# Performance work log

Hardware: AMD Instinct MI355X
Metric: run time of the kernel (lower is better)

The kernel has to match this reference:

```python
import jax, jax.numpy as jnp
import numpy as np

EPS = 1e-5

def rmsnorm(x, g):
    var = jnp.mean(jnp.square(x), axis=-1, keepdims=True)
    return x * jax.lax.rsqrt(var + EPS) * g

def setup_inputs() -> dict:
    key = jax.random.key(0)
    ks = jax.random.split(key, 8)
    B, S, T, D = 2, 2048, 2048, 1024
    H, HKV, HD = 16, 4, 64
    std = 0.02
    return {
        "x": jax.random.normal(ks[0], (B, S, D), jnp.float32),
        "kv": jax.random.normal(ks[1], (B, T, D), jnp.float32),
        "wq": jax.random.normal(ks[2], (H * HD, D), jnp.float32) * std,
        "wk": jax.random.normal(ks[3], (HKV * HD, D), jnp.float32) * std,
        "wv": jax.random.normal(ks[4], (HKV * HD, D), jnp.float32) * std,
        "wo": jax.random.normal(ks[5], (D, H * HD), jnp.float32) * std,
        "gq": jnp.ones((D,), jnp.float32),
        "gkv": jnp.ones((D,), jnp.float32),
    }

def reference(x, kv, wq, wk, wv, wo, gq, gkv):
    B, S, D = x.shape
    T = kv.shape[1]
    H, HKV, HD = 16, 4, 64
    R = H // HKV  # heads per kv group
    xn = rmsnorm(x, gq)
    kvn = rmsnorm(kv, gkv)
    # projections
    q = (xn @ wq.T).reshape(B, S, HKV, R, HD)   # grouped query heads
    k = (kvn @ wk.T).reshape(B, T, HKV, HD)
    v = (kvn @ wv.T).reshape(B, T, HKV, HD)
    scale = 1.0 / jnp.sqrt(jnp.float32(HD))
    # block-mask is None -> full dense cross attention; GQA via broadcast einsum
    scores = jnp.einsum('bsgrd,btgd->bgrst', q, k) * scale  # [B,HKV,R,S,T]
    probs = jax.nn.softmax(scores, axis=-1)
    out = jnp.einsum('bgrst,btgd->bsgrd', probs, v)  # [B,S,HKV,R,HD]
    out = out.reshape(B, S, H * HD) @ wo.T
    return x + out
```

## Files before the change

### kernel.cpp

```cpp
#include <hip/hip_runtime.h>

#define DEV __device__ __forceinline__

typedef __attribute__((ext_vector_type(8))) short frag8;
typedef __attribute__((ext_vector_type(8))) _Float16 h8;
typedef __attribute__((ext_vector_type(4))) float f32x4;

DEV unsigned short f2bf(float f) {
  union { float f; unsigned int u; } v; v.f = f;
  unsigned int r = v.u + 0x7fffu + ((v.u >> 16) & 1u);
  return (unsigned short)(r >> 16);
}

DEV unsigned short f2h(float f) {
  union { _Float16 h[2]; unsigned short u[2]; } v;
  v.h[0] = (_Float16)f;
  return v.u[0];
}

DEV float h2f(unsigned short u) {
  union { _Float16 h[2]; unsigned short u[2]; } v;
  v.u[0] = u;
  return (float)v.h[0];
}

DEV unsigned int pack2h(float a, float b) {
  union { __fp16 __attribute__((ext_vector_type(2))) p; unsigned int u; } v;
  v.p = __builtin_amdgcn_cvt_pkrtz(a, b);
  return v.u;
}

DEV void async_load16(const void* g, void* l) {
  __builtin_amdgcn_global_load_lds(
      (const __attribute__((address_space(1))) void*)g,
      (__attribute__((address_space(3))) void*)l,
      16, 0, 0);
}

__global__ __launch_bounds__(256) void fused_cast(const float* __restrict__ wq,
                                                  const float* __restrict__ wk,
                                                  const float* __restrict__ wv,
                                                  const float* __restrict__ wo,
                                                  unsigned short* __restrict__ wqb,
                                                  unsigned short* __restrict__ wkvb,
                                                  unsigned short* __restrict__ wob,
                                                  float qscale) {
  const int b = blockIdx.x;
  const float* src;
  unsigned short* dst;
  float sc = 1.0f;
  int base;
  if (b < 1024) { src = wq; dst = wqb; sc = qscale; base = b; }
  else if (b < 1280) { src = wk; dst = wkvb; base = b - 1024; }
  else if (b < 1536) { src = wv; dst = wkvb + 262144; base = b - 1280; }
  else { src = wo; dst = wob; base = b - 1536; }
  const int i = (base * 256 + threadIdx.x) * 4;
  float4 v = *(const float4*)&src[i];
  ushort4 o;
  o.x = f2bf(v.x * sc); o.y = f2bf(v.y * sc);
  o.z = f2bf(v.z * sc); o.w = f2bf(v.w * sc);
  *(ushort4*)&dst[i] = o;
}

__global__ __launch_bounds__(256) void rmsnorm2(const float* __restrict__ x,
                                                const float* __restrict__ kv,
                                                const float* __restrict__ gq,
                                                const float* __restrict__ gkv,
                                                unsigned short* __restrict__ xn,
                                                unsigned short* __restrict__ kvn) {
  int row = blockIdx.x;
  const int tid = threadIdx.x;
  const float* src;
  const float* g;
  unsigned short* dst;
  if (row < 4096) { src = x; g = gq; dst = xn; }
  else { row -= 4096; src = kv; g = gkv; dst = kvn; }
  const float* xr = src + (size_t)row * 1024;
  float4 v = *(const float4*)&xr[tid * 4];
  float ss = v.x * v.x + v.y * v.y + v.z * v.z + v.w * v.w;
  ss += __shfl_xor(ss, 32); ss += __shfl_xor(ss, 16);
  ss += __shfl_xor(ss, 8);  ss += __shfl_xor(ss, 4);
  ss += __shfl_xor(ss, 2);  ss += __shfl_xor(ss, 1);
  __shared__ float red[4];
  if ((tid & 63) == 0) red[tid >> 6] = ss;
  __syncthreads();
  float tot = red[0] + red[1] + red[2] + red[3];
  float inv = rsqrtf(tot * (1.0f / 1024.0f) + 1e-5f);
  float4 gv = *(const float4*)&g[tid * 4];
  ushort4 o;
  o.x = f2bf(v.x * inv * gv.x); o.y = f2bf(v.y * inv * gv.y);
  o.z = f2bf(v.z * inv * gv.z); o.w = f2bf(v.w * inv * gv.w);
  *(ushort4*)&dst[(size_t)row * 1024 + tid * 4] = o;
}

template <int BM, int BN, int MODE>
__global__ __launch_bounds__(256) void gemm_bt(const unsigned short* __restrict__ A,
                                               const unsigned short* __restrict__ W,
                                               void* __restrict__ out,
                                               const float* __restrict__ resid,
                                               unsigned short* __restrict__ out2,
                                               int M, int N, int K) {
  constexpr int MI = BM / 32, NI = BN / 32;
  constexpr int PA = BM / 32, PB = BN / 32;
  __shared__ unsigned short Al[2][2][BM * 32];
  __shared__ unsigned short Bl[2][2][BN * 32];
  const int tid = threadIdx.x;
  const int w = tid >> 6, l = tid & 63;
  const int quad = l >> 4, ln = l & 15;
  const int m0 = blockIdx.y * BM, n0 = blockIdx.x * BN;
  const int wm0 = (w >> 1) * (MI * 16), wn0 = (w & 1) * (NI * 16);
  const int r4 = l >> 2;
  const int c4 = (l & 3) * 8;

  f32x4 acc[MI][NI] = {};

  auto stage = [&](int buf, int kk) {
#pragma unroll
    for (int j = 0; j < PA; ++j) {
      const int idx = w * PA + j;
      const int p = idx / (BM / 16), c = idx % (BM / 16);
      async_load16(A + (size_t)(m0 + c * 16 + r4) * K + kk + p * 32 + c4,
                   &Al[buf][p][c * 512]);
    }
#pragma unroll
    for (int j = 0; j < PB; ++j) {
      const int idx = w * PB + j;
      const int p = idx / (BN / 16), c = idx % (BN / 16);
      async_load16(W + (size_t)(n0 + c * 16 + r4) * K + kk + p * 32 + c4,
                   &Bl[buf][p][c * 512]);
    }
  };

  stage(0, 0);
  const int iters = K >> 6;
#pragma unroll 2
  for (int it = 0; it < iters; ++it) {
    const int buf = it & 1;
    __syncthreads();
    if (it + 1 < iters) stage(buf ^ 1, (it + 1) << 6);
#pragma unroll
    for (int kc = 0; kc < 2; ++kc) {
      frag8 af[MI], bfr[NI];
#pragma unroll
      for (int mi = 0; mi < MI; ++mi)
        af[mi] = *(const frag8*)&Al[buf][kc][(wm0 + mi * 16 + ln) * 32 + quad * 8];
#pragma unroll
      for (int ni = 0; ni < NI; ++ni)
        bfr[ni] = *(const frag8*)&Bl[buf][kc][(wn0 + ni * 16 + ln) * 32 + quad * 8];
#pragma unroll
      for (int mi = 0; mi < MI; ++mi)
#pragma unroll
        for (int ni = 0; ni < NI; ++ni)
          acc[mi][ni] = __builtin_amdgcn_mfma_f32_16x16x32_bf16(af[mi], bfr[ni], acc[mi][ni], 0, 0, 0);
    }
  }

#pragma unroll
  for (int mi = 0; mi < MI; ++mi) {
#pragma unroll
    for (int ni = 0; ni < NI; ++ni) {
#pragma unroll
      for (int r = 0; r < 4; ++r) {
        const int row = m0 + wm0 + mi * 16 + quad * 4 + r;
        const int col = n0 + wn0 + ni * 16 + ln;
        const float v = acc[mi][ni][r];
        if (MODE == 0) {
          ((unsigned short*)out)[(size_t)row * N + col] = f2bf(v);
        } else if (MODE == 2) {
          const size_t idx = (size_t)row * N + col;
          ((float*)out)[idx] = resid[idx] + v;
        } else {
          if (col < 256) {
            ((unsigned short*)out)[(size_t)row * 256 + col] = f2bf(v);
          } else {
            const int c2 = col - 256, gg = c2 >> 6, dd = c2 & 63;
            const int bb = row >> 11, t = row & 2047;
            out2[((size_t)((bb * 4 + gg) * 64 + dd) << 11) + t] = f2h(v);
          }
        }
      }
    }
  }
}

__global__ __launch_bounds__(256, 4) void flash_attn(const unsigned short* __restrict__ q,
                                                     const unsigned short* __restrict__ k,
                                                     const unsigned short* __restrict__ vT,
                                                     unsigned short* __restrict__ o0,
                                                     unsigned short* __restrict__ o1,
                                                     float* __restrict__ l0p,
                                                     float* __restrict__ l1p) {
  __shared__ unsigned short KV[4][64 * 32];
  __shared__ unsigned short P[4 * 32 * 72];

  const int tid = threadIdx.x;
  const int w = tid >> 6, l = tid & 63;
  const int quad = l >> 4, ln = l & 15;
  const int s0 = blockIdx.x * 128;
  const int h = blockIdx.y, g = h >> 2;
  const int b = blockIdx.z >> 1, ts = blockIdx.z & 1;
  const int tbase = ts << 10;

  unsigned short* Opart = ts ? o1 : o0;
  float* lpart = ts ? l1p : l0p;

  frag8 qf[2][2];
#pragma unroll
  for (int nq = 0; nq < 2; ++nq)
#pragma unroll
    for (int c = 0; c < 2; ++c)
      qf[nq][c] = *(const frag8*)&q[(((size_t)(b * 2048 + s0 + w * 32 + nq * 16 + ln)) << 10) +
                                    h * 64 + c * 32 + quad * 8];

  f32x4 oacc[2][4] = {};
  float lsum[2] = {0.0f, 0.0f};

  const unsigned short* kbase = k + ((size_t)(b * 2048)) * 256 + g * 64;
  const unsigned short* vbase = vT + (((size_t)(b * 4 + g) * 64) << 11);
  unsigned short* Pw = &P[w * 32 * 72];

  const int r4 = l >> 2;
  const int c4 = (l & 3) * 8;

  for (int it = 0; it < 16; ++it) {
    const int t0 = tbase + it * 64;
    __syncthreads();
#pragma unroll
    for (int c = 0; c < 4; ++c) {
      const unsigned short* src;
      if (w < 2)
        src = kbase + (size_t)(t0 + c * 16 + r4) * 256 + w * 32 + c4;
      else
        src = vbase + (((size_t)(c * 16 + r4)) << 11) + t0 + (w - 2) * 32 + c4;
      async_load16(src, &KV[w][c * 512]);
    }
    __syncthreads();

    f32x4 st[2][4];
#pragma unroll
    for (int tb = 0; tb < 4; ++tb) {
      frag8 ka = *(const frag8*)&KV[0][(tb * 16 + ln) * 32 + quad * 8];
      frag8 kb2 = *(const frag8*)&KV[1][(tb * 16 + ln) * 32 + quad * 8];
#pragma unroll
      for (int nq = 0; nq < 2; ++nq) {
        f32x4 s = {};
        s = __builtin_amdgcn_mfma_f32_16x16x32_bf16(ka, qf[nq][0], s, 0, 0, 0);
        s = __builtin_amdgcn_mfma_f32_16x16x32_bf16(kb2, qf[nq][1], s, 0, 0, 0);
        st[nq][tb] = s;
      }
    }

#pragma unroll
    for (int nq = 0; nq < 2; ++nq) {
#pragma unroll
      for (int tb = 0; tb < 4; ++tb) {
        float p0 = __builtin_amdgcn_exp2f(fminf(st[nq][tb][0], 14.0f));
        float p1 = __builtin_amdgcn_exp2f(fminf(st[nq][tb][1], 14.0f));
        float p2 = __builtin_amdgcn_exp2f(fminf(st[nq][tb][2], 14.0f));
        float p3 = __builtin_amdgcn_exp2f(fminf(st[nq][tb][3], 14.0f));
        lsum[nq] += (p0 + p1) + (p2 + p3);
        uint2 pk; pk.x = pack2h(p0, p1); pk.y = pack2h(p2, p3);
        *(uint2*)&Pw[(nq * 16 + ln) * 72 + tb * 16 + quad * 4] = pk;
      }
    }

    asm volatile("s_waitcnt lgkmcnt(0)" ::: "memory");

#pragma unroll
    for (int c = 0; c < 2; ++c) {
      h8 pf0 = *(const h8*)&Pw[(0 * 16 + ln) * 72 + c * 32 + quad * 8];
      h8 pf1 = *(const h8*)&Pw[(1 * 16 + ln) * 72 + c * 32 + quad * 8];
#pragma unroll
      for (int cb = 0; cb < 4; ++cb) {
        h8 vb = *(const h8*)&KV[2 + c][(cb * 16 + ln) * 32 + quad * 8];
        oacc[0][cb] = __builtin_amdgcn_mfma_f32_16x16x32_f16(pf0, vb, oacc[0][cb], 0, 0, 0);
        oacc[1][cb] = __builtin_amdgcn_mfma_f32_16x16x32_f16(pf1, vb, oacc[1][cb], 0, 0, 0);
      }
    }
  }

#pragma unroll
  for (int nq = 0; nq < 2; ++nq) {
    lsum[nq] += __shfl_xor(lsum[nq], 16);
    lsum[nq] += __shfl_xor(lsum[nq], 32);
    if (l < 16)
      lpart[(size_t)(b * 2048 + s0 + w * 32 + nq * 16 + l) * 16 + h] = lsum[nq];
#pragma unroll
    for (int r = 0; r < 4; ++r) {
      const size_t row = (size_t)(b * 2048 + s0 + w * 32 + nq * 16 + quad * 4 + r);
#pragma unroll
      for (int cb = 0; cb < 4; ++cb)
        Opart[(row << 10) + h * 64 + cb * 16 + ln] = f2h(oacc[nq][cb][r]);
    }
  }
}

__global__ __launch_bounds__(256) void combine(const unsigned short* __restrict__ O0,
                                               const unsigned short* __restrict__ O1,
                                               const float* __restrict__ l0p,
                                               const float* __restrict__ l1p,
                                               unsigned short* __restrict__ att) {
  const int row = blockIdx.x, tid = threadIdx.x;
  const int col = tid * 4;
  const int h = tid >> 4;
  const float inv = 1.0f / (l0p[row * 16 + h] + l1p[row * 16 + h]);
  const size_t idx = ((size_t)row << 10) + col;
  ushort4 a = *(const ushort4*)&O0[idx];
  ushort4 b = *(const ushort4*)&O1[idx];
  ushort4 o;
  o.x = f2bf((h2f(a.x) + h2f(b.x)) * inv);
  o.y = f2bf((h2f(a.y) + h2f(b.y)) * inv);
  o.z = f2bf((h2f(a.z) + h2f(b.z)) * inv);
  o.w = f2bf((h2f(a.w) + h2f(b.w)) * inv);
  *(ushort4*)&att[idx] = o;
}

extern "C" void kernel_launch(void* const* d_in, const int* in_sizes, int n_in,
                              void* d_out, int out_size, void* d_ws, size_t ws_size,
                              hipStream_t stream) {
  const float* x   = (const float*)d_in[0];
  const float* kv  = (const float*)d_in[1];
  const float* wq  = (const float*)d_in[2];
  const float* wk  = (const float*)d_in[3];
  const float* wv  = (const float*)d_in[4];
  const float* wo  = (const float*)d_in[5];
  const float* gq  = (const float*)d_in[6];
  const float* gkv = (const float*)d_in[7];

  char* ws = (char*)d_ws;
  unsigned short* xn   = (unsigned short*)(ws);
  unsigned short* kvn  = (unsigned short*)(ws + 8388608);
  unsigned short* qb   = (unsigned short*)(ws + 16777216);
  unsigned short* kb   = (unsigned short*)(ws + 25165824);
  unsigned short* vTb  = (unsigned short*)(ws + 27262976);
  unsigned short* attb = (unsigned short*)(ws + 29360128);
  unsigned short* wqb  = (unsigned short*)(ws + 37748736);
  unsigned short* wkvb = (unsigned short*)(ws + 39845888);
  unsigned short* wob  = (unsigned short*)(ws + 40894464);
  unsigned short* Opart0 = xn;
  unsigned short* Opart1 = kvn;
  float* l0p = (float*)wqb;
  float* l1p = (float*)(ws + 37748736 + 262144);

  const float qscale = 0.18033688011112042f;
  fused_cast<<<2560, 256, 0, stream>>>(wq, wk, wv, wo, wqb, wkvb, wob, qscale);
  rmsnorm2<<<8192, 256, 0, stream>>>(x, kv, gq, gkv, xn, kvn);

  gemm_bt<64, 64, 0><<<dim3(16, 64), 256, 0, stream>>>(xn, wqb, qb, nullptr, nullptr,
                                                       4096, 1024, 1024);
  gemm_bt<64, 64, 3><<<dim3(8, 64), 256, 0, stream>>>(kvn, wkvb, kb, nullptr, vTb,
                                                      4096, 512, 1024);

  flash_attn<<<dim3(16, 16, 4), 256, 0, stream>>>(qb, kb, vTb, Opart0, Opart1, l0p, l1p);
  combine<<<4096, 256, 0, stream>>>(Opart0, Opart1, l0p, l1p, attb);

  gemm_bt<64, 64, 2><<<dim3(16, 64), 256, 0, stream>>>(attb, wob, d_out, x, nullptr,
                                                       4096, 1024, 1024);
}
```

Measured before the change: 204.1 us.

## Split-K 128x128 projection GEMMs with fp16 partials and larger flash-attention query tiles

Replaces the 64x64 Q and output projection GEMMs with a 128x128-tile split-K kernel. Each half of K writes fp16 partials; the Q partials are summed inside the attention prologue and the output partials are summed in a new residual-add kernel. K is now stored as fp16, and the QK^T MFMAs switch from bf16 to f16. Flash attention now processes 256 query rows per block, 64 per wave, with the exp applied directly after each score MFMA, and its occupancy hint drops from 4 to 2. The larger tiles aim to raise data reuse, but they cost an extra combine pass, a single-buffered GEMM main loop, fewer resident blocks, and a small loss of precision from the fp16 partial sums.

```diff
diff --git a/kernel.cpp b/kernel.cpp
--- a/kernel.cpp
+++ b/kernel.cpp
@@ -93,97 +93,139 @@
   *(ushort4*)&dst[(size_t)row * 1024 + tid * 4] = o;
 }
 
-template <int BM, int BN, int MODE>
-__global__ __launch_bounds__(256) void gemm_bt(const unsigned short* __restrict__ A,
+__global__ __launch_bounds__(256) void gemm_fat(const unsigned short* __restrict__ A,
+                                                const unsigned short* __restrict__ W,
+                                                unsigned short* __restrict__ p0,
+                                                unsigned short* __restrict__ p1) {
+  __shared__ unsigned short Al[2][128 * 32];
+  __shared__ unsigned short Bl[2][128 * 32];
+  const int tid = threadIdx.x;
+  const int w = tid >> 6, l = tid & 63;
+  const int quad = l >> 4, ln = l & 15;
+  const int m0 = blockIdx.y * 128, n0 = blockIdx.x * 128;
+  const int kb0 = blockIdx.z * 512;
+  unsigned short* part = blockIdx.z ? p1 : p0;
+  const int wm0 = (w >> 1) * 64, wn0 = (w & 1) * 64;
+  const int r4 = l >> 2;
+  const int c4 = (l & 3) * 8;
+
+  f32x4 acc[4][4] = {};
+
+  for (int kk = 0; kk < 512; kk += 64) {
+    __syncthreads();
+#pragma unroll
+    for (int j = 0; j < 4; ++j) {
+      const int idx = w * 4 + j;
+      const int p = idx >> 3, rb = (idx & 7) * 16;
+      async_load16(A + (size_t)(m0 + rb + r4) * 1024 + kb0 + kk + p * 32 + c4,
+                   &Al[p][rb * 32]);
+      async_load16(W + (size_t)(n0 + rb + r4) * 1024 + kb0 + kk + p * 32 + c4,
+                   &Bl[p][rb * 32]);
+    }
+    __syncthreads();
+#pragma unroll
+    for (int kc = 0; kc < 2; ++kc) {
+      frag8 af[4], bf[4];
+#pragma unroll
+      for (int mi = 0; mi < 4; ++mi)
+        af[mi] = *(const frag8*)&Al[kc][(wm0 + mi * 16 + ln) * 32 + quad * 8];
+#pragma unroll
+      for (int ni = 0; ni < 4; ++ni)
+        bf[ni] = *(const frag8*)&Bl[kc][(wn0 + ni * 16 + ln) * 32 + quad * 8];
+#pragma unroll
+      for (int mi = 0; mi < 4; ++mi)
+#pragma unroll
+        for (int ni = 0; ni < 4; ++ni)
+          acc[mi][ni] = __builtin_amdgcn_mfma_f32_16x16x32_bf16(af[mi], bf[ni], acc[mi][ni], 0, 0, 0);
+    }
+  }
+
+#pragma unroll
+  for (int mi = 0; mi < 4; ++mi)
+#pragma unroll
+    for (int ni = 0; ni < 4; ++ni)
+#pragma unroll
+      for (int r = 0; r < 4; ++r) {
+        const int row = m0 + wm0 + mi * 16 + quad * 4 + r;
+        const int col = n0 + wn0 + ni * 16 + ln;
+        part[((size_t)row << 10) + col] = f2h(acc[mi][ni][r]);
+      }
+}
+
+__global__ __launch_bounds__(256) void gemm_kv(const unsigned short* __restrict__ A,
                                                const unsigned short* __restrict__ W,
-                                               void* __restrict__ out,
-                                               const float* __restrict__ resid,
-                                               unsigned short* __restrict__ out2,
-                                               int M, int N, int K) {
-  constexpr int MI = BM / 32, NI = BN / 32;
-  constexpr int PA = BM / 32, PB = BN / 32;
+                                               unsigned short* __restrict__ kout,
+                                               unsigned short* __restrict__ vout) {
+  constexpr int BM = 64, BN = 64;
   __shared__ unsigned short Al[2][2][BM * 32];
   __shared__ unsigned short Bl[2][2][BN * 32];
   const int tid = threadIdx.x;
   const int w = tid >> 6, l = tid & 63;
   const int quad = l >> 4, ln = l & 15;
   const int m0 = blockIdx.y * BM, n0 = blockIdx.x * BN;
-  const int wm0 = (w >> 1) * (MI * 16), wn0 = (w & 1) * (NI * 16);
+  const int wm0 = (w >> 1) * 32, wn0 = (w & 1) * 32;
   const int r4 = l >> 2;
   const int c4 = (l & 3) * 8;
-
-  f32x4 acc[MI][NI] = {};
+  const int K = 1024;
+
+  f32x4 acc[2][2] = {};
 
   auto stage = [&](int buf, int kk) {
 #pragma unroll
-    for (int j = 0; j < PA; ++j) {
-      const int idx = w * PA + j;
-      const int p = idx / (BM / 16), c = idx % (BM / 16);
+    for (int j = 0; j < 2; ++j) {
+      const int idx = w * 2 + j;
+      const int p = idx >> 2, c = idx & 3;
       async_load16(A + (size_t)(m0 + c * 16 + r4) * K + kk + p * 32 + c4,
                    &Al[buf][p][c * 512]);
-    }
-#pragma unroll
-    for (int j = 0; j < PB; ++j) {
-      const int idx = w * PB + j;
-      const int p = idx / (BN / 16), c = idx % (BN / 16);
       async_load16(W + (size_t)(n0 + c * 16 + r4) * K + kk + p * 32 + c4,
                    &Bl[buf][p][c * 512]);
     }
   };
 
   stage(0, 0);
-  const int iters = K >> 6;
 #pragma unroll 2
-  for (int it = 0; it < iters; ++it) {
+  for (int it = 0; it < 16; ++it) {
     const int buf = it & 1;
     __syncthreads();
-    if (it + 1 < iters) stage(buf ^ 1, (it + 1) << 6);
+    if (it < 15) stage(buf ^ 1, (it + 1) << 6);
 #pragma unroll
     for (int kc = 0; kc < 2; ++kc) {
-      frag8 af[MI], bfr[NI];
-#pragma unroll
-      for (int mi = 0; mi < MI; ++mi)
+      frag8 af[2], bf[2];
+#pragma unroll
+      for (int mi = 0; mi < 2; ++mi)
         af[mi] = *(const frag8*)&Al[buf][kc][(wm0 + mi * 16 + ln) * 32 + quad * 8];
 #pragma unroll
-      for (int ni = 0; ni < NI; ++ni)
-        bfr[ni] = *(const frag8*)&Bl[buf][kc][(wn0 + ni * 16 + ln) * 32 + quad * 8];
-#pragma unroll
-      for (int mi = 0; mi < MI; ++mi)
-#pragma unroll
-        for (int ni = 0; ni < NI; ++ni)
-          acc[mi][ni] = __builtin_amdgcn_mfma_f32_16x16x32_bf16(af[mi], bfr[ni], acc[mi][ni], 0, 0, 0);
+      for (int ni = 0; ni < 2; ++ni)
+        bf[ni] = *(const frag8*)&Bl[buf][kc][(wn0 + ni * 16 + ln) * 32 + quad * 8];
+#pragma unroll
+      for (int mi = 0; mi < 2; ++mi)
+#pragma unroll
+        for (int ni = 0; ni < 2; ++ni)
+          acc[mi][ni] = __builtin_amdgcn_mfma_f32_16x16x32_bf16(af[mi], bf[ni], acc[mi][ni], 0, 0, 0);
     }
   }
 
 #pragma unroll
-  for (int mi = 0; mi < MI; ++mi) {
-#pragma unroll
-    for (int ni = 0; ni < NI; ++ni) {
+  for (int mi = 0; mi < 2; ++mi)
+#pragma unroll
+    for (int ni = 0; ni < 2; ++ni)
 #pragma unroll
       for (int r = 0; r < 4; ++r) {
         const int row = m0 + wm0 + mi * 16 + quad * 4 + r;
         const int col = n0 + wn0 + ni * 16 + ln;
         const float v = acc[mi][ni][r];
-        if (MODE == 0) {
-          ((unsigned short*)out)[(size_t)row * N + col] = f2bf(v);
-        } else if (MODE == 2) {
-          const size_t idx = (size_t)row * N + col;
-          ((float*)out)[idx] = resid[idx] + v;
+        if (col < 256) {
+          kout[(size_t)row * 256 + col] = f2h(v);
         } else {
-          if (col < 256) {
-            ((unsigned short*)out)[(size_t)row * 256 + col] = f2bf(v);
-          } else {
-            const int c2 = col - 256, gg = c2 >> 6, dd = c2 & 63;
-            const int bb = row >> 11, t = row & 2047;
-            out2[((size_t)((bb * 4 + gg) * 64 + dd) << 11) + t] = f2h(v);
-          }
+          const int c2 = col - 256, gg = c2 >> 6, dd = c2 & 63;
+          const int bb = row >> 11, t = row & 2047;
+          vout[((size_t)((bb * 4 + gg) * 64 + dd) << 11) + t] = f2h(v);
         }
       }
-    }
-  }
-}
-
-__global__ __launch_bounds__(256, 4) void flash_attn(const unsigned short* __restrict__ q,
+}
+
+__global__ __launch_bounds__(256, 2) void flash_attn(const unsigned short* __restrict__ qp0,
+                                                     const unsigned short* __restrict__ qp1,
                                                      const unsigned short* __restrict__ k,
                                                      const unsigned short* __restrict__ vT,
                                                      unsigned short* __restrict__ o0,
@@ -191,12 +233,12 @@
                                                      float* __restrict__ l0p,
                                                      float* __restrict__ l1p) {
   __shared__ unsigned short KV[4][64 * 32];
-  __shared__ unsigned short P[4 * 32 * 72];
+  __shared__ unsigned short P[4 * 64 * 72];
 
   const int tid = threadIdx.x;
   const int w = tid >> 6, l = tid & 63;
   const int quad = l >> 4, ln = l & 15;
-  const int s0 = blockIdx.x * 128;
+  const int s0 = blockIdx.x * 256;
   const int h = blockIdx.y, g = h >> 2;
   const int b = blockIdx.z >> 1, ts = blockIdx.z & 1;
   const int tbase = ts << 10;
@@ -204,20 +246,22 @@
   unsigned short* Opart = ts ? o1 : o0;
   float* lpart = ts ? l1p : l0p;
 
-  frag8 qf[2][2];
-#pragma unroll
-  for (int nq = 0; nq < 2; ++nq)
-#pragma unroll
-    for (int c = 0; c < 2; ++c)
-      qf[nq][c] = *(const frag8*)&q[(((size_t)(b * 2048 + s0 + w * 32 + nq * 16 + ln)) << 10) +
-                                    h * 64 + c * 32 + quad * 8];
-
-  f32x4 oacc[2][4] = {};
-  float lsum[2] = {0.0f, 0.0f};
+  h8 qf[4][2];
+#pragma unroll
+  for (int nq = 0; nq < 4; ++nq)
+#pragma unroll
+    for (int c = 0; c < 2; ++c) {
+      const size_t off = (((size_t)(b * 2048 + s0 + w * 64 + nq * 16 + ln)) << 10) +
+                         h * 64 + c * 32 + quad * 8;
+      qf[nq][c] = *(const h8*)&qp0[off] + *(const h8*)&qp1[off];
+    }
+
+  f32x4 oacc[4][4] = {};
+  float lsum[4] = {0.0f, 0.0f, 0.0f, 0.0f};
 
   const unsigned short* kbase = k + ((size_t)(b * 2048)) * 256 + g * 64;
   const unsigned short* vbase = vT + (((size_t)(b * 4 + g) * 64) << 11);
-  unsigned short* Pw = &P[w * 32 * 72];
+  unsigned short* Pw = &P[w * 64 * 72];
 
   const int r4 = l >> 2;
   const int c4 = (l & 3) * 8;
@@ -236,28 +280,19 @@
     }
     __syncthreads();
 
-    f32x4 st[2][4];
 #pragma unroll
     for (int tb = 0; tb < 4; ++tb) {
-      frag8 ka = *(const frag8*)&KV[0][(tb * 16 + ln) * 32 + quad * 8];
-      frag8 kb2 = *(const frag8*)&KV[1][(tb * 16 + ln) * 32 + quad * 8];
-#pragma unroll
-      for (int nq = 0; nq < 2; ++nq) {
+      h8 ka = *(const h8*)&KV[0][(tb * 16 + ln) * 32 + quad * 8];
+      h8 kb2 = *(const h8*)&KV[1][(tb * 16 + ln) * 32 + quad * 8];
+#pragma unroll
+      for (int nq = 0; nq < 4; ++nq) {
         f32x4 s = {};
-        s = __builtin_amdgcn_mfma_f32_16x16x32_bf16(ka, qf[nq][0], s, 0, 0, 0);
-        s = __builtin_amdgcn_mfma_f32_16x16x32_bf16(kb2, qf[nq][1], s, 0, 0, 0);
-        st[nq][tb] = s;
-      }
-    }
-
-#pragma unroll
-    for (int nq = 0; nq < 2; ++nq) {
-#pragma unroll
-      for (int tb = 0; tb < 4; ++tb) {
-        float p0 = __builtin_amdgcn_exp2f(fminf(st[nq][tb][0], 14.0f));
-        float p1 = __builtin_amdgcn_exp2f(fminf(st[nq][tb][1], 14.0f));
-        float p2 = __builtin_amdgcn_exp2f(fminf(st[nq][tb][2], 14.0f));
-        float p3 = __builtin_amdgcn_exp2f(fminf(st[nq][tb][3], 14.0f));
+        s = __builtin_amdgcn_mfma_f32_16x16x32_f16(ka, qf[nq][0], s, 0, 0, 0);
+        s = __builtin_amdgcn_mfma_f32_16x16x32_f16(kb2, qf[nq][1], s, 0, 0, 0);
+        float p0 = __builtin_amdgcn_exp2f(fminf(s[0], 14.0f));
+        float p1 = __builtin_amdgcn_exp2f(fminf(s[1], 14.0f));
+        float p2 = __builtin_amdgcn_exp2f(fminf(s[2], 14.0f));
+        float p3 = __builtin_amdgcn_exp2f(fminf(s[3], 14.0f));
         lsum[nq] += (p0 + p1) + (p2 + p3);
         uint2 pk; pk.x = pack2h(p0, p1); pk.y = pack2h(p2, p3);
         *(uint2*)&Pw[(nq * 16 + ln) * 72 + tb * 16 + quad * 4] = pk;
@@ -268,26 +303,29 @@
 
 #pragma unroll
     for (int c = 0; c < 2; ++c) {
-      h8 pf0 = *(const h8*)&Pw[(0 * 16 + ln) * 72 + c * 32 + quad * 8];
-      h8 pf1 = *(const h8*)&Pw[(1 * 16 + ln) * 72 + c * 32 + quad * 8];
+      h8 pf[4];
+#pragma unroll
+      for (int nq = 0; nq < 4; ++nq)
+        pf[nq] = *(const h8*)&Pw[(nq * 16 + ln) * 72 + c * 32 + quad * 8];
 #pragma unroll
       for (int cb = 0; cb < 4; ++cb) {
         h8 vb = *(const h8*)&KV[2 + c][(cb * 16 + ln) * 32 + quad * 8];
-        oacc[0][cb] = __builtin_amdgcn_mfma_f32_16x16x32_f16(pf0, vb, oacc[0][cb], 0, 0, 0);
-        oacc[1][cb] = __builtin_amdgcn_mfma_f32_16x16x32_f16(pf1, vb, oacc[1][cb], 0, 0, 0);
+#pragma unroll
+        for (int nq = 0; nq < 4; ++nq)
+          oacc[nq][cb] = __builtin_amdgcn_mfma_f32_16x16x32_f16(pf[nq], vb, oacc[nq][cb], 0, 0, 0);
       }
     }
   }
 
 #pragma unroll
-  for (int nq = 0; nq < 2; ++nq) {
+  for (int nq = 0; nq < 4; ++nq) {
     lsum[nq] += __shfl_xor(lsum[nq], 16);
     lsum[nq] += __shfl_xor(lsum[nq], 32);
     if (l < 16)
-      lpart[(size_t)(b * 2048 + s0 + w * 32 + nq * 16 + l) * 16 + h] = lsum[nq];
+      lpart[(size_t)(b * 2048 + s0 + w * 64 + nq * 16 + l) * 16 + h] = lsum[nq];
 #pragma unroll
     for (int r = 0; r < 4; ++r) {
-      const size_t row = (size_t)(b * 2048 + s0 + w * 32 + nq * 16 + quad * 4 + r);
+      const size_t row = (size_t)(b * 2048 + s0 + w * 64 + nq * 16 + quad * 4 + r);
 #pragma unroll
       for (int cb = 0; cb < 4; ++cb)
         Opart[(row << 10) + h * 64 + cb * 16 + ln] = f2h(oacc[nq][cb][r]);
@@ -315,6 +353,23 @@
   *(ushort4*)&att[idx] = o;
 }
 
+__global__ __launch_bounds__(256) void o_combine(const float* __restrict__ x,
+                                                 const unsigned short* __restrict__ p0,
+                                                 const unsigned short* __restrict__ p1,
+                                                 float* __restrict__ out) {
+  const int row = blockIdx.x, tid = threadIdx.x;
+  const size_t idx = ((size_t)row << 10) + tid * 4;
+  float4 xv = *(const float4*)&x[idx];
+  ushort4 a = *(const ushort4*)&p0[idx];
+  ushort4 b = *(const ushort4*)&p1[idx];
+  float4 o;
+  o.x = xv.x + h2f(a.x) + h2f(b.x);
+  o.y = xv.y + h2f(a.y) + h2f(b.y);
+  o.z = xv.z + h2f(a.z) + h2f(b.z);
+  o.w = xv.w + h2f(a.w) + h2f(b.w);
+  *(float4*)&out[idx] = o;
+}
+
 extern "C" void kernel_launch(void* const* d_in, const int* in_sizes, int n_in,
                               void* d_out, int out_size, void* d_ws, size_t ws_size,
                               hipStream_t stream) {
@@ -328,17 +383,20 @@
   const float* gkv = (const float*)d_in[7];
 
   char* ws = (char*)d_ws;
-  unsigned short* xn   = (unsigned short*)(ws);
-  unsigned short* kvn  = (unsigned short*)(ws + 8388608);
-  unsigned short* qb   = (unsigned short*)(ws + 16777216);
-  unsigned short* kb   = (unsigned short*)(ws + 25165824);
-  unsigned short* vTb  = (unsigned short*)(ws + 27262976);
-  unsigned short* attb = (unsigned short*)(ws + 29360128);
-  unsigned short* wqb  = (unsigned short*)(ws + 37748736);
-  unsigned short* wkvb = (unsigned short*)(ws + 39845888);
-  unsigned short* wob  = (unsigned short*)(ws + 40894464);
+  unsigned short* xn    = (unsigned short*)(ws);
+  unsigned short* kvn   = (unsigned short*)(ws + 8388608);
+  unsigned short* qpart0= (unsigned short*)(ws + 16777216);
+  unsigned short* kb    = (unsigned short*)(ws + 25165824);
+  unsigned short* vTb   = (unsigned short*)(ws + 27262976);
+  unsigned short* qpart1= (unsigned short*)(ws + 29360128);
+  unsigned short* attb  = (unsigned short*)(ws + 29360128);
+  unsigned short* wqb   = (unsigned short*)(ws + 37748736);
+  unsigned short* wkvb  = (unsigned short*)(ws + 39845888);
+  unsigned short* wob   = (unsigned short*)(ws + 40894464);
   unsigned short* Opart0 = xn;
   unsigned short* Opart1 = kvn;
+  unsigned short* opart0 = xn;
+  unsigned short* opart1 = kvn;
   float* l0p = (float*)wqb;
   float* l1p = (float*)(ws + 37748736 + 262144);
 
@@ -346,14 +404,13 @@
   fused_cast<<<2560, 256, 0, stream>>>(wq, wk, wv, wo, wqb, wkvb, wob, qscale);
   rmsnorm2<<<8192, 256, 0, stream>>>(x, kv, gq, gkv, xn, kvn);
 
-  gemm_bt<64, 64, 0><<<dim3(16, 64), 256, 0, stream>>>(xn, wqb, qb, nullptr, nullptr,
-                                                       4096, 1024, 1024);
-  gemm_bt<64, 64, 3><<<dim3(8, 64), 256, 0, stream>>>(kvn, wkvb, kb, nullptr, vTb,
-                                                      4096, 512, 1024);
-
-  flash_attn<<<dim3(16, 16, 4), 256, 0, stream>>>(qb, kb, vTb, Opart0, Opart1, l0p, l1p);
+  gemm_fat<<<dim3(8, 32, 2), 256, 0, stream>>>(xn, wqb, qpart0, qpart1);
+  gemm_kv<<<dim3(8, 64), 256, 0, stream>>>(kvn, wkvb, kb, vTb);
+
+  flash_attn<<<dim3(8, 16, 4), 256, 0, stream>>>(qpart0, qpart1, kb, vTb,
+                                                 Opart0, Opart1, l0p, l1p);
   combine<<<4096, 256, 0, stream>>>(Opart0, Opart1, l0p, l1p, attb);
 
-  gemm_bt<64, 64, 2><<<dim3(16, 64), 256, 0, stream>>>(attb, wob, d_out, x, nullptr,
-                                                       4096, 1024, 1024);
-}
+  gemm_fat<<<dim3(8, 32, 2), 256, 0, stream>>>(attb, wob, opart0, opart1);
+  o_combine<<<4096, 256, 0, stream>>>(x, opart0, opart1, (float*)d_out);
+}
```

Result: slower. 218.1 us (+6.9%).
